# Optimization experiments

Measured on AMD Instinct MI355X. Metric: run time of the kernel, lower is better.

The kernel has to match this reference:

```python
import jax, jax.numpy as jnp
import numpy as np

N = 8192
DISCO_LAMBDA = 0.1
DCORR_POWER = 2  # static, from __init__


def setup_inputs() -> dict:
    key = jax.random.key(0)
    k1, k2, k3, k4 = jax.random.split(key, 4)
    inferences = jax.random.uniform(k1, (N,), dtype=jnp.float32, minval=1e-6, maxval=1.0 - 1e-6)
    labels = jax.random.randint(k2, (N,), 0, 2, dtype=jnp.int32)
    disco_target = jax.random.normal(k3, (N,), dtype=jnp.float32)
    weights = jax.random.uniform(k4, (N,), dtype=jnp.float32)
    return {"inferences": inferences, "labels": labels,
            "disco_target": disco_target, "weights": weights}


def _bce(p, y, w):
    # torch F.binary_cross_entropy: clamps log terms at -100, mean reduction
    logp = jnp.clip(jnp.log(p), -100.0)
    log1mp = jnp.clip(jnp.log1p(-p), -100.0)
    return jnp.mean(w * -(y * logp + (1.0 - y) * log1mp))


def _dcorr(v1, v2, w, mask):
    # mask selects labels==0 subset; zero weights + divide by subset count
    # reproduces torch means over the fancy-indexed subset exactly.
    nf = jnp.sum(mask)                      # subset size (traced scalar)
    wm = w * mask                           # [N]
    amat = jnp.abs(v1[:, None] - v1[None, :])   # [N,N]
    bmat = jnp.abs(v2[:, None] - v2[None, :])   # [N,N]
    a_row = (amat @ wm) / nf                # weighted row means
    b_row = (bmat @ wm) / nf
    a_tot = jnp.dot(a_row, wm) / nf
    b_tot = jnp.dot(b_row, wm) / nf
    Amat = amat - a_row[None, :] - a_row[:, None] + a_tot  # double-centered
    Bmat = bmat - b_row[None, :] - b_row[:, None] + b_tot
    AB = jnp.dot((Amat * Bmat) @ wm, wm) / (nf * nf)
    AA = jnp.dot((Amat * Amat) @ wm, wm) / (nf * nf)
    BB = jnp.dot((Bmat * Bmat) @ wm, wm) / (nf * nf)
    if DCORR_POWER == 1:
        return AB / jnp.sqrt(AA * BB)
    elif DCORR_POWER == 2:
        return AB ** 2 / (AA * BB)
    else:
        return (AB / jnp.sqrt(AA * BB)) ** DCORR_POWER


def reference(inferences, labels, disco_target, weights):
    y = labels.astype(inferences.dtype)
    bce = _bce(inferences, y, weights)
    mask = (labels == 0).astype(inferences.dtype)
    dcorr = _dcorr(inferences, disco_target, weights, mask)
    total = bce + DISCO_LAMBDA * dcorr
    return (total, bce, DISCO_LAMBDA * dcorr)
```

## Files before the change

kernel.cpp:

```cpp
#include <hip/hip_runtime.h>
#include <math.h>

constexpr int N_ELEM = 8192;
constexpr int BLK    = 256;
constexpr int WAVES  = 4;
constexpr int RPW    = 4;
constexpr int RPB    = WAVES * RPW;
constexpr int KP_GRID = N_ELEM / RPB;
constexpr int CHUNK  = 512;
constexpr int NCHUNK = N_ELEM / CHUNK;
constexpr int BLKF   = 1024;
constexpr float LAMBDA = 0.1f;


__global__ void __launch_bounds__(BLK) kp_pairs(
        const float* __restrict__ inf, const int* __restrict__ lab,
        const float* __restrict__ tgt, const float* __restrict__ wt,
        double* __restrict__ gpart) {
    __shared__ float4 sc[2][CHUNK];
    __shared__ double sred[WAVES][6];
    const int tx = threadIdx.x, lane = tx & 63, wid = tx >> 6;
    const int r0 = blockIdx.x * RPB + wid * RPW;

    float x[RPW], y[RPW], u[RPW];
#pragma unroll
    for (int r = 0; r < RPW; ++r) {
        x[r] = inf[r0 + r];
        y[r] = tgt[r0 + r];
        u[r] = (lab[r0 + r] == 0) ? wt[r0 + r] : 0.0f;
    }
    float ra[RPW] = {}, rb[RPW] = {}, pp[RPW] = {};

#pragma unroll
    for (int s = 0; s < CHUNK / BLK; ++s) {
        int j = s * BLK + tx;
        float wmj = (lab[j] == 0) ? wt[j] : 0.0f;
        sc[0][j] = make_float4(inf[j], tgt[j], wmj, 0.0f);
    }
    __syncthreads();

    for (int ch = 0; ch < NCHUNK; ++ch) {
        const int cur = ch & 1;
        const int chn = (ch + 1) & (NCHUNK - 1);
        const int jb  = chn * CHUNK + tx;
        float p0n = inf[jb],       t0n = tgt[jb],       w0n = wt[jb];
        float p1n = inf[jb + BLK], t1n = tgt[jb + BLK], w1n = wt[jb + BLK];
        int   l0n = lab[jb],       l1n = lab[jb + BLK];

#pragma unroll
        for (int s = 0; s < CHUNK / 64; ++s) {
            float4 cj = sc[cur][s * 64 + lane];
#pragma unroll
            for (int r = 0; r < RPW; ++r) {
                float fa = fabsf(x[r] - cj.x);
                float fb = fabsf(y[r] - cj.y);
                ra[r] = fmaf(cj.z, fa, ra[r]);
                rb[r] = fmaf(cj.z, fb, rb[r]);
                pp[r] = fmaf(cj.z, fa * fb, pp[r]);
            }
        }
        if (ch + 1 < NCHUNK) {
            sc[cur ^ 1][tx]       = make_float4(p0n, t0n, (l0n == 0) ? w0n : 0.0f, 0.0f);
            sc[cur ^ 1][BLK + tx] = make_float4(p1n, t1n, (l1n == 0) ? w1n : 0.0f, 0.0f);
        }
        __syncthreads();
    }

#pragma unroll
    for (int r = 0; r < RPW; ++r) {
#pragma unroll
        for (int d = 32; d > 0; d >>= 1) {
            ra[r] += __shfl_xor(ra[r], d);
            rb[r] += __shfl_xor(rb[r], d);
            pp[r] += __shfl_xor(pp[r], d);
        }
    }
    if (lane == 0) {
        double s0 = 0, s1 = 0, s2 = 0, s3 = 0, s4 = 0, s5 = 0;
#pragma unroll
        for (int r = 0; r < RPW; ++r) {
            double U = (double)u[r];
            double A = (double)ra[r], B = (double)rb[r], Pp = (double)pp[r];
            s0 += U * Pp;
            s1 += U * A;  s2 += U * A * A;
            s3 += U * B;  s4 += U * B * B;
            s5 += U * A * B;
        }
        sred[wid][0] = s0; sred[wid][1] = s1; sred[wid][2] = s2;
        sred[wid][3] = s3; sred[wid][4] = s4; sred[wid][5] = s5;
    }
    __syncthreads();
    if (tx == 0) {
        double* g = gpart + (size_t)blockIdx.x * 6;
#pragma unroll
        for (int k = 0; k < 6; ++k)
            g[k] = sred[0][k] + sred[1][k] + sred[2][k] + sred[3][k];
    }
}

__global__ void __launch_bounds__(BLKF) kf_final(
        const float* __restrict__ inf, const int* __restrict__ lab,
        const float* __restrict__ tgt, const float* __restrict__ wt,
        const double* __restrict__ gpart, float* __restrict__ out) {
    __shared__ float  redM[BLKF / 64][8];
    __shared__ double redG[BLKF / 64][6];
    int tx = threadIdx.x, lane = tx & 63, wid = tx >> 6;

    float vb = 0.f, vn = 0.f, vw = 0.f, v1a = 0.f, v2a = 0.f, v1b = 0.f, v2b = 0.f;
#pragma unroll
    for (int k = 0; k < N_ELEM / BLKF; ++k) {
        int i = k * BLKF + tx;
        float p = inf[i];
        int   y = lab[i];
        float w = wt[i];
        float t = tgt[i];
        float logp   = fmaxf(logf(p),    -100.0f);
        float log1mp = fmaxf(log1pf(-p), -100.0f);
        float yf = (float)y;
        vb += w * -(yf * logp + (1.0f - yf) * log1mp);
        bool  m  = (y == 0);
        float mf = m ? 1.0f : 0.0f;
        float wm = m ? w : 0.0f;
        vn += mf; vw += wm;
        v1a += wm * p; v2a += wm * p * p;
        v1b += wm * t; v2b += wm * t * t;
    }
    float vm[7] = {vb, vn, vw, v1a, v2a, v1b, v2b};
#pragma unroll
    for (int k = 0; k < 7; ++k) {
        float s = vm[k];
#pragma unroll
        for (int d = 32; d > 0; d >>= 1) s += __shfl_xor(s, d);
        if (lane == 0) redM[wid][k] = s;
    }

    double a0 = 0, a1 = 0, a2 = 0, a3 = 0, a4 = 0, a5 = 0;
    if (tx < KP_GRID) {
        const double* g = gpart + (size_t)tx * 6;
        a0 = g[0]; a1 = g[1]; a2 = g[2]; a3 = g[3]; a4 = g[4]; a5 = g[5];
    }
#pragma unroll
    for (int d = 32; d > 0; d >>= 1) {
        a0 += __shfl_xor(a0, d); a1 += __shfl_xor(a1, d); a2 += __shfl_xor(a2, d);
        a3 += __shfl_xor(a3, d); a4 += __shfl_xor(a4, d); a5 += __shfl_xor(a5, d);
    }
    if (lane == 0) {
        redG[wid][0] = a0; redG[wid][1] = a1; redG[wid][2] = a2;
        redG[wid][3] = a3; redG[wid][4] = a4; redG[wid][5] = a5;
    }
    __syncthreads();

    if (tx == 0) {
        double M[7] = {0, 0, 0, 0, 0, 0, 0};
        double G[6] = {0, 0, 0, 0, 0, 0};
        for (int wv = 0; wv < BLKF / 64; ++wv) {
#pragma unroll
            for (int k = 0; k < 7; ++k) M[k] += (double)redM[wv][k];
#pragma unroll
            for (int k = 0; k < 6; ++k) G[k] += redG[wv][k];
        }
        double bceS = M[0], NF = M[1], W = M[2];
        double S1a = M[3], S2a = M[4], S1b = M[5], S2b = M[6];
        double P = G[0], Ra1 = G[1], Ra2 = G[2], Rb1 = G[3], Rb2 = G[4], Rab = G[5];

        double in1 = 1.0 / NF;
        double in2 = in1 * in1, in3 = in2 * in1, in4 = in2 * in2;

        double AAa = 2.0 * (W * S2a - S1a * S1a)
                   - 4.0 * Ra2 * in1 + 2.0 * W * Ra2 * in2
                   + 4.0 * Ra1 * Ra1 * in2 - 4.0 * W * Ra1 * Ra1 * in3
                   + W * W * Ra1 * Ra1 * in4;
        double BBa = 2.0 * (W * S2b - S1b * S1b)
                   - 4.0 * Rb2 * in1 + 2.0 * W * Rb2 * in2
                   + 4.0 * Rb1 * Rb1 * in2 - 4.0 * W * Rb1 * Rb1 * in3
                   + W * W * Rb1 * Rb1 * in4;
        double ABa = P
                   - 4.0 * Rab * in1 + 2.0 * W * Rab * in2
                   + 4.0 * Ra1 * Rb1 * in2 - 4.0 * W * Ra1 * Rb1 * in3
                   + W * W * Ra1 * Rb1 * in4;

        double AB = ABa * in2, AA = AAa * in2, BB = BBa * in2;
        double dcorr = (AB * AB) / (AA * BB);
        double ld = (double)LAMBDA * dcorr;
        double bce = bceS / (double)N_ELEM;
        out[0] = (float)(bce + ld);
        out[1] = (float)bce;
        out[2] = (float)ld;
    }
}

extern "C" void kernel_launch(void* const* d_in, const int* in_sizes, int n_in,
                              void* d_out, int out_size, void* d_ws, size_t ws_size,
                              hipStream_t stream) {
    const float* inf = (const float*)d_in[0];
    const int*   lab = (const int*)d_in[1];
    const float* tgt = (const float*)d_in[2];
    const float* wt  = (const float*)d_in[3];
    float* out = (float*)d_out;
    double* gpart = (double*)d_ws;

    kp_pairs<<<KP_GRID, BLK, 0, stream>>>(inf, lab, tgt, wt, gpart);
    kf_final<<<1, BLKF, 0, stream>>>(inf, lab, tgt, wt, gpart, out);
}
```

Measured before the change: 87.97 us.

## Compact label-zero elements first and skip pairwise work for masked rows

Adds a compaction kernel that scatters the label-zero elements, packed as float4 (p, t, masked weight), to the front of a workspace buffer and writes their count. The pairwise kernel then runs only over the compacted rows and columns, exiting early for blocks beyond the count and shortening the chunk loop, which roughly halves the O(N^2) work for random labels. This costs an extra kernel launch and a redundant per-block global prefix count over all labels. Loads also become single float4 reads instead of four scalar arrays.

```diff
diff --git a/kernel.cpp b/kernel.cpp
--- a/kernel.cpp
+++ b/kernel.cpp
@@ -8,44 +8,98 @@
 constexpr int RPB    = WAVES * RPW;
 constexpr int KP_GRID = N_ELEM / RPB;
 constexpr int CHUNK  = 512;
-constexpr int NCHUNK = N_ELEM / CHUNK;
 constexpr int BLKF   = 1024;
 constexpr float LAMBDA = 0.1f;
 
-
-__global__ void __launch_bounds__(BLK) kp_pairs(
+constexpr size_t OFF_CNT = 24576;
+
+__global__ void __launch_bounds__(BLK) k1_compact(
         const float* __restrict__ inf, const int* __restrict__ lab,
         const float* __restrict__ tgt, const float* __restrict__ wt,
+        float4* __restrict__ c, int* __restrict__ pcnt) {
+    __shared__ int swc[WAVES];
+    __shared__ int r2[WAVES][2];
+    const int tx = threadIdx.x, lane = tx & 63, wid = tx >> 6;
+    const int blockStart = blockIdx.x * BLK;
+    const int i = blockStart + tx;
+
+    float p = inf[i], t = tgt[i], w = wt[i];
+    bool  m = (lab[i] == 0);
+
+    int czb = 0, czt = 0;
+    for (int k = tx; k < N_ELEM; k += BLK) {
+        int z = (lab[k] == 0) ? 1 : 0;
+        czt += z;
+        czb += (k < blockStart) ? z : 0;
+    }
+#pragma unroll
+    for (int d = 32; d > 0; d >>= 1) {
+        czb += __shfl_xor(czb, d);
+        czt += __shfl_xor(czt, d);
+    }
+
+    unsigned long long bal = __ballot(m);
+    int pz  = __popcll(bal & ((1ull << lane) - 1ull));
+    int wzc = __popcll(bal);
+
+    if (lane == 0) { swc[wid] = wzc; r2[wid][0] = czb; r2[wid][1] = czt; }
+    __syncthreads();
+
+    int zb = 0;
+#pragma unroll
+    for (int v = 0; v < WAVES; ++v) zb += (v < wid) ? swc[v] : 0;
+    int gzb = r2[0][0] + r2[1][0] + r2[2][0] + r2[3][0];
+    int gzt = r2[0][1] + r2[1][1] + r2[2][1] + r2[3][1];
+
+    int pos;
+    if (m) {
+        pos = gzb + zb + pz;
+    } else {
+        int nzb_global = blockStart - gzb;
+        int nzb_wave   = wid * 64 - zb;
+        int nz_lane    = lane - pz;
+        pos = N_ELEM - 1 - (nzb_global + nzb_wave + nz_lane);
+    }
+    c[pos] = make_float4(p, t, m ? w : 0.0f, 0.0f);
+
+    if (blockIdx.x == 0 && tx == 0) *pcnt = gzt;
+}
+
+__global__ void __launch_bounds__(BLK) kp_pairs(
+        const float4* __restrict__ c, const int* __restrict__ pcnt,
         double* __restrict__ gpart) {
     __shared__ float4 sc[2][CHUNK];
     __shared__ double sred[WAVES][6];
     const int tx = threadIdx.x, lane = tx & 63, wid = tx >> 6;
-    const int r0 = blockIdx.x * RPB + wid * RPW;
+    const int cnt = *pcnt;
+    const int nActive = (cnt + RPB - 1) / RPB;
+    double* g = gpart + (size_t)blockIdx.x * 6;
+
+    if ((int)blockIdx.x >= nActive) {
+        if (tx == 0) { g[0] = 0; g[1] = 0; g[2] = 0; g[3] = 0; g[4] = 0; g[5] = 0; }
+        return;
+    }
+    const int nch = (cnt + CHUNK - 1) / CHUNK;
+    const int r0  = blockIdx.x * RPB + wid * RPW;
 
     float x[RPW], y[RPW], u[RPW];
 #pragma unroll
     for (int r = 0; r < RPW; ++r) {
-        x[r] = inf[r0 + r];
-        y[r] = tgt[r0 + r];
-        u[r] = (lab[r0 + r] == 0) ? wt[r0 + r] : 0.0f;
+        float4 cr = c[r0 + r];
+        x[r] = cr.x; y[r] = cr.y; u[r] = cr.z;
     }
     float ra[RPW] = {}, rb[RPW] = {}, pp[RPW] = {};
 
-#pragma unroll
-    for (int s = 0; s < CHUNK / BLK; ++s) {
-        int j = s * BLK + tx;
-        float wmj = (lab[j] == 0) ? wt[j] : 0.0f;
-        sc[0][j] = make_float4(inf[j], tgt[j], wmj, 0.0f);
-    }
-    __syncthreads();
-
-    for (int ch = 0; ch < NCHUNK; ++ch) {
+    sc[0][tx]       = c[tx];
+    sc[0][BLK + tx] = c[BLK + tx];
+    __syncthreads();
+
+    for (int ch = 0; ch < nch; ++ch) {
         const int cur = ch & 1;
-        const int chn = (ch + 1) & (NCHUNK - 1);
+        const int chn = (ch + 1 < nch) ? ch + 1 : nch - 1;
         const int jb  = chn * CHUNK + tx;
-        float p0n = inf[jb],       t0n = tgt[jb],       w0n = wt[jb];
-        float p1n = inf[jb + BLK], t1n = tgt[jb + BLK], w1n = wt[jb + BLK];
-        int   l0n = lab[jb],       l1n = lab[jb + BLK];
+        float4 n0 = c[jb];
+        float4 n1 = c[jb + BLK];
 
 #pragma unroll
         for (int s = 0; s < CHUNK / 64; ++s) {
@@ -59,9 +113,9 @@
                 pp[r] = fmaf(cj.z, fa * fb, pp[r]);
             }
         }
-        if (ch + 1 < NCHUNK) {
-            sc[cur ^ 1][tx]       = make_float4(p0n, t0n, (l0n == 0) ? w0n : 0.0f, 0.0f);
-            sc[cur ^ 1][BLK + tx] = make_float4(p1n, t1n, (l1n == 0) ? w1n : 0.0f, 0.0f);
+        if (ch + 1 < nch) {
+            sc[cur ^ 1][tx]       = n0;
+            sc[cur ^ 1][BLK + tx] = n1;
         }
         __syncthreads();
     }
@@ -91,7 +145,6 @@
     }
     __syncthreads();
     if (tx == 0) {
-        double* g = gpart + (size_t)blockIdx.x * 6;
 #pragma unroll
         for (int k = 0; k < 6; ++k)
             g[k] = sred[0][k] + sred[1][k] + sred[2][k] + sred[3][k];
@@ -136,8 +189,8 @@
 
     double a0 = 0, a1 = 0, a2 = 0, a3 = 0, a4 = 0, a5 = 0;
     if (tx < KP_GRID) {
-        const double* g = gpart + (size_t)tx * 6;
-        a0 = g[0]; a1 = g[1]; a2 = g[2]; a3 = g[3]; a4 = g[4]; a5 = g[5];
+        const double* gr = gpart + (size_t)tx * 6;
+        a0 = gr[0]; a1 = gr[1]; a2 = gr[2]; a3 = gr[3]; a4 = gr[4]; a5 = gr[5];
     }
 #pragma unroll
     for (int d = 32; d > 0; d >>= 1) {
@@ -197,8 +250,12 @@
     const float* tgt = (const float*)d_in[2];
     const float* wt  = (const float*)d_in[3];
     float* out = (float*)d_out;
+
     double* gpart = (double*)d_ws;
-
-    kp_pairs<<<KP_GRID, BLK, 0, stream>>>(inf, lab, tgt, wt, gpart);
+    int*    pcnt  = (int*)((char*)d_ws + OFF_CNT);
+    float4* c     = (float4*)((char*)d_ws + OFF_CNT + 256);
+
+    k1_compact<<<N_ELEM / BLK, BLK, 0, stream>>>(inf, lab, tgt, wt, c, pcnt);
+    kp_pairs<<<KP_GRID, BLK, 0, stream>>>(c, pcnt, gpart);
     kf_final<<<1, BLKF, 0, stream>>>(inf, lab, tgt, wt, gpart, out);
 }
```

New measurement: 85.25 us. 1.03x faster.
